# Optimization experiments

Measured on AMD Instinct MI355X. Metric: run time of the kernel, lower is better.

## Reference

```python
import jax, jax.numpy as jnp
import numpy as np

N = 100000      # nodes
E = 800000      # edges
IN = 32         # in_channels (one-hot width)
HID = 32        # hidden_channels per head
HEADS = 4
OUT = 10        # out_channels
G = 64          # graphs in batch
NEG_SLOPE = 0.2


def setup_inputs() -> dict:
    key = jax.random.key(0)
    ks = jax.random.split(key, 12)
    s = 0.1
    D = HEADS * HID  # 128
    return {
        "x": jax.random.randint(ks[0], (N,), 0, IN),
        "edge_index": jax.random.randint(ks[1], (2, E), 0, N),
        "batch": jnp.sort(jax.random.randint(ks[2], (N,), 0, G)),
        # conv1: IN -> HEADS x HID
        "W1": jax.random.normal(ks[3], (IN, D), jnp.float32) * s,
        "att_src1": jax.random.normal(ks[4], (HEADS, HID), jnp.float32) * s,
        "att_dst1": jax.random.normal(ks[5], (HEADS, HID), jnp.float32) * s,
        "b1": jnp.zeros((D,), jnp.float32),
        # conv3: D -> HEADS x HID
        "W3": jax.random.normal(ks[6], (D, D), jnp.float32) * s,
        "att_src3": jax.random.normal(ks[7], (HEADS, HID), jnp.float32) * s,
        "att_dst3": jax.random.normal(ks[8], (HEADS, HID), jnp.float32) * s,
        "b3": jnp.zeros((D,), jnp.float32),
        # final classifier
        "lin_w": jax.random.normal(ks[9], (D, OUT), jnp.float32) * s,
        "lin_b": jnp.zeros((OUT,), jnp.float32),
    }


def gat_conv(h, src, dst, W, att_src, att_dst, bias):
    """PyG GATConv (concat=True, add_self_loops already in src/dst)."""
    n = h.shape[0]
    hproj = (h @ W).reshape(n, HEADS, -1)                 # [N,H,C]
    a_src = jnp.einsum("nhc,hc->nh", hproj, att_src)      # [N,H]
    a_dst = jnp.einsum("nhc,hc->nh", hproj, att_dst)
    e = a_src[src] + a_dst[dst]                           # [E',H]
    e = jnp.where(e >= 0, e, NEG_SLOPE * e)               # LeakyReLU(0.2)
    # segment softmax over incoming edges of each destination node
    m = jax.ops.segment_max(e, dst, num_segments=n)       # [N,H]
    ex = jnp.exp(e - m[dst])
    denom = jax.ops.segment_sum(ex, dst, num_segments=n)  # [N,H]
    alpha = ex / denom[dst]                               # [E',H]
    msg = alpha[:, :, None] * hproj[src]                  # [E',H,C]
    out = jax.ops.segment_sum(msg, dst, num_segments=n)   # [N,H,C]
    return out.reshape(n, -1) + bias


def reference(x, edge_index, batch, W1, att_src1, att_dst1, b1,
              W3, att_src3, att_dst3, b3, lin_w, lin_b):
    # add self-loops once (PyG GATConv default add_self_loops=True)
    loop = jnp.arange(N, dtype=edge_index.dtype)
    src = jnp.concatenate([edge_index[0], loop])
    dst = jnp.concatenate([edge_index[1], loop])

    h = jax.nn.one_hot(x, IN, dtype=jnp.float32)          # [N,IN]
    h = jax.nn.relu(gat_conv(h, src, dst, W1, att_src1, att_dst1, b1))
    h = gat_conv(h, src, dst, W3, att_src3, att_dst3, b3)  # [N,D]

    # global_mean_pool over graph ids
    sums = jax.ops.segment_sum(h, batch, num_segments=G)   # [G,D]
    cnt = jax.ops.segment_sum(jnp.ones((N,), h.dtype), batch, num_segments=G)
    pooled = sums / jnp.maximum(cnt, 1.0)[:, None]
    return pooled @ lin_w + lin_b                          # [G,OUT]
```

## Files before the change

kernel.cpp:

```cpp
#include <hip/hip_runtime.h>
#include <hip/hip_fp16.h>

#define HEADS 4
#define HID 32
#define DCH 128
#define OUTC 10
#define NSLOPE 0.2f

#define SCAN_T 256
#define SCAN_PT 8
#define SCAN_ELEMS (SCAN_T * SCAN_PT)

#define POOL_BLOCKS 2048
#define BN1 64
#define SC_TILES 256

__global__ void k_deg(const int* __restrict__ esrc, const int* __restrict__ edst,
                      const int* __restrict__ x, int E, int N,
                      int* __restrict__ deg, unsigned short* __restrict__ rank) {
    int e = blockIdx.x * blockDim.x + threadIdx.x;
    int EP = E + N;
    if (e >= EP) return;
    int s, d;
    if (e < E) { s = esrc[e]; d = edst[e]; } else { s = e - E; d = s; }
    int r = atomicAdd(&deg[d], 1);
    rank[e] = (unsigned short)((r << 5) | x[s]);
}

__global__ void k_scan_a(const int* __restrict__ deg, int* __restrict__ rowstart,
                         int* __restrict__ bsum, int N) {
    __shared__ int sh[SCAN_T];
    int base = blockIdx.x * SCAN_ELEMS;
    int t = threadIdx.x;
    int v[SCAN_PT];
    int s = 0;
#pragma unroll
    for (int i = 0; i < SCAN_PT; i++) {
        int idx = base + t * SCAN_PT + i;
        int dv = (idx < N) ? deg[idx] : 0;
        s += dv; v[i] = s;
    }
    sh[t] = s;
    __syncthreads();
    for (int off = 1; off < SCAN_T; off <<= 1) {
        int add = (t >= off) ? sh[t - off] : 0;
        __syncthreads();
        sh[t] += add;
        __syncthreads();
    }
    int excl = (t > 0) ? sh[t - 1] : 0;
#pragma unroll
    for (int i = 0; i < SCAN_PT; i++) {
        int idx = base + t * SCAN_PT + i;
        if (idx < N) rowstart[idx + 1] = v[i] + excl;
    }
    if (t == SCAN_T - 1) bsum[blockIdx.x] = sh[t];
}

__global__ void k_scanb_tables(int* __restrict__ bsum, int nb,
        const float* __restrict__ W1, const float* __restrict__ as1, const float* __restrict__ ad1,
        const float* __restrict__ W3, const float* __restrict__ as3, const float* __restrict__ ad3,
        float* __restrict__ EXPT2, float* __restrict__ was3, float* __restrict__ wad3) {
    if (blockIdx.x == 0) {
        __shared__ int sh[1024];
        int t = threadIdx.x;
        sh[t] = (t < nb) ? bsum[t] : 0;
        __syncthreads();
        for (int off = 1; off < 1024; off <<= 1) {
            int add = (t >= off) ? sh[t - off] : 0;
            __syncthreads();
            sh[t] += add;
            __syncthreads();
        }
        if (t < nb) bsum[t] = (t > 0) ? sh[t - 1] : 0;
    } else {
        __shared__ float ts[32][HEADS], td[32][HEADS];
        int t = threadIdx.x;
        if (t < 128) {
            int cs = t >> 2, h = t & 3;
            const float* w = W1 + cs * DCH + h * HID;
            const float* a = as1 + h * HID;
            const float* b = ad1 + h * HID;
            float s1 = 0.f, s2 = 0.f;
#pragma unroll
            for (int j = 0; j < HID; j++) { float wv = w[j]; s1 = fmaf(wv, a[j], s1); s2 = fmaf(wv, b[j], s2); }
            ts[cs][h] = s1; td[cs][h] = s2;
        }
        __syncthreads();
        if (t < 128) {
            int h = t >> 5, cs = t & 31;
            for (int cd = 0; cd < 32; cd++) {
                float ev = ts[cs][h] + td[cd][h];
                ev = ev >= 0.f ? ev : NSLOPE * ev;
                EXPT2[cd * DCH + t] = __expf(ev);
            }
            for (int hh = 0; hh < HEADS; hh++) {
                const float* wr = W3 + (size_t)t * DCH + hh * HID;
                const float* a = as3 + hh * HID;
                const float* b = ad3 + hh * HID;
                float s1 = 0.f, s2 = 0.f;
#pragma unroll
                for (int j = 0; j < HID; j++) { float wv = wr[j]; s1 = fmaf(wv, a[j], s1); s2 = fmaf(wv, b[j], s2); }
                was3[hh * DCH + t] = s1; wad3[hh * DCH + t] = s2;
            }
        }
    }
}

__global__ void k_scan_c_bounds(int* __restrict__ rowstart, const int* __restrict__ boff,
                                const int* __restrict__ batch, int* __restrict__ gstart,
                                float* __restrict__ pool, int N, int G) {
    int i = blockIdx.x * blockDim.x + threadIdx.x;
    if (i < G * DCH) pool[i] = 0.f;
    if (i < N) {
        rowstart[i + 1] += boff[i / SCAN_ELEMS];
        if (i == 0) rowstart[0] = 0;
    }
    if (i > N) return;
    if (i == 0) {
        int b0 = batch[0];
        for (int g = 0; g <= b0; g++) gstart[g] = 0;
    } else if (i == N) {
        int bl = batch[N - 1];
        for (int g = bl + 1; g <= G; g++) gstart[g] = N;
    } else {
        int b = batch[i], bp = batch[i - 1];
        for (int g = bp + 1; g <= b; g++) gstart[g] = i;
    }
}

__global__ void k_scatter3(const int* __restrict__ esrc, const int* __restrict__ edst,
                           int E, int N, const int* __restrict__ rowstart,
                           const unsigned short* __restrict__ rank,
                           int* __restrict__ csr) {
    int rng  = blockIdx.x & 7;
    int tile = blockIdx.x >> 3;
    int ntiles = gridDim.x >> 3;
    int lo = rng * (N >> 3);
    int hi = (rng == 7) ? N : lo + (N >> 3);
    int EP = E + N;
    int stride = ntiles * blockDim.x;
    for (int e = tile * blockDim.x + threadIdx.x; e < EP; e += stride) {
        int s, d;
        if (e < E) { s = esrc[e]; d = edst[e]; } else { s = e - E; d = s; }
        if (d < lo || d >= hi) continue;
        unsigned short rk = rank[e];
        int pos = rowstart[d] + (rk >> 5);
        csr[pos] = (s << 5) | (rk & 31);
    }
}

__global__ __launch_bounds__(512) void k_conv1b(
        const int* __restrict__ rowstart, const int* __restrict__ csr,
        const int* __restrict__ x, const float* __restrict__ W1,
        const float* __restrict__ EXPT2, const float* __restrict__ b1,
        const float* __restrict__ was3, const float* __restrict__ wad3,
        __half* __restrict__ h1, float* __restrict__ asrc, float* __restrict__ adst,
        int N) {
    __shared__ float El[32 * 132 + 1];
    __shared__ int   hist[BN1][33];
    __shared__ int   xdl[BN1];
    int t = threadIdx.x;
    int r0 = blockIdx.x * BN1;
    for (int i = t; i < 32 * DCH; i += 512) {
        int cd = i >> 7, rem = i & 127;
        int hh = rem >> 5, kk = rem & 31;
        El[cd * 132 + hh * 33 + kk] = EXPT2[i];
    }
    for (int i = t; i < BN1 * 33; i += 512) ((int*)hist)[i] = 0;
    if (t < BN1) {
        int node = r0 + t;
        xdl[t] = (node < N) ? x[node] : 0;
    }
    __syncthreads();
    {
        int ln = t >> 3, sub = t & 7;
        int node = r0 + ln;
        if (node < N) {
            int p0 = rowstart[node], p1 = rowstart[node + 1];
            for (int p = p0 + sub; p < p1; p += 8)
                atomicAdd(&hist[ln][csr[p] & 31], 1);
        }
    }
    __syncthreads();
    int ct = t & 31, rt = t >> 5;
    int h = ct >> 3;
    float acc[4][4], den[4];
#pragma unroll
    for (int r = 0; r < 4; r++) { den[r] = 0.f;
#pragma unroll
        for (int j = 0; j < 4; j++) acc[r][j] = 0.f; }
#pragma unroll 4
    for (int k = 0; k < 32; k++) {
        float4 wv = *(const float4*)&W1[k * DCH + 4 * ct];
#pragma unroll
        for (int r = 0; r < 4; r++) {
            int row = rt * 4 + r;
            float g = (float)hist[row][k] * El[xdl[row] * 132 + h * 33 + k];
            den[r] += g;
            acc[r][0] = fmaf(g, wv.x, acc[r][0]);
            acc[r][1] = fmaf(g, wv.y, acc[r][1]);
            acc[r][2] = fmaf(g, wv.z, acc[r][2]);
            acc[r][3] = fmaf(g, wv.w, acc[r][3]);
        }
    }
    float4 bb = *(const float4*)&b1[4 * ct];
    float bbv[4] = {bb.x, bb.y, bb.z, bb.w};
#pragma unroll
    for (int r = 0; r < 4; r++) {
        float inv = 1.0f / den[r];
#pragma unroll
        for (int j = 0; j < 4; j++) {
            float v = acc[r][j] * inv + bbv[j];
            acc[r][j] = v > 0.f ? v : 0.f;
        }
        int row = r0 + rt * 4 + r;
        if (row < N) {
            union { __half hh[4]; uint2 u; } pk;
#pragma unroll
            for (int j = 0; j < 4; j++) pk.hh[j] = __float2half(acc[r][j]);
            *(uint2*)&h1[(size_t)row * DCH + 4 * ct] = pk.u;
        }
    }
    float4 ws = *(const float4*)&was3[h * DCH + 4 * ct];
    float4 wd = *(const float4*)&wad3[h * DCH + 4 * ct];
#pragma unroll
    for (int r = 0; r < 4; r++) {
        float ps = acc[r][0] * ws.x + acc[r][1] * ws.y + acc[r][2] * ws.z + acc[r][3] * ws.w;
        float pd = acc[r][0] * wd.x + acc[r][1] * wd.y + acc[r][2] * wd.z + acc[r][3] * wd.w;
        ps += __shfl_xor(ps, 1);  pd += __shfl_xor(pd, 1);
        ps += __shfl_xor(ps, 2);  pd += __shfl_xor(pd, 2);
        ps += __shfl_xor(ps, 4);  pd += __shfl_xor(pd, 4);
        int row = r0 + rt * 4 + r;
        if ((ct & 7) == 0 && row < N) {
            asrc[row * HEADS + h] = ps;
            adst[row * HEADS + h] = pd;
        }
    }
}

__global__ __launch_bounds__(256) void k_gather3w(
        const int* __restrict__ rowstart, const int* __restrict__ csr,
        const __half* __restrict__ hp, const float* __restrict__ asrc,
        const float* __restrict__ adst, __half* __restrict__ z, int N) {
    int t = threadIdx.x;
    int wid = t >> 6, lane = t & 63;
    int d = blockIdx.x * 4 + wid;
    if (d >= N) return;
    int lane16 = lane & 15, grp = lane >> 4;
    int myh = lane16 >> 2;
    float adst_h = adst[d * HEADS + myh];
    int p0 = rowstart[d], p1 = rowstart[d + 1];
    float a[8], b[8];
#pragma unroll
    for (int j = 0; j < 8; j++) { a[j] = 0.f; b[j] = 0.f; }
    float dena = 0.f, denb = 0.f;
    int p = p0 + grp;
    for (; p + 4 < p1; p += 8) {
        int s0 = csr[p] >> 5;
        int s1 = csr[p + 4] >> 5;
        float ev0 = asrc[s0 * HEADS + myh] + adst_h;
        float ev1 = asrc[s1 * HEADS + myh] + adst_h;
        ev0 = ev0 >= 0.f ? ev0 : NSLOPE * ev0;
        ev1 = ev1 >= 0.f ? ev1 : NSLOPE * ev1;
        float ex0 = __expf(ev0);
        float ex1 = __expf(ev1);
        dena += ex0; denb += ex1;
        const uint4 r0v = *(const uint4*)(hp + (size_t)s0 * DCH + lane16 * 8);
        const uint4 r1v = *(const uint4*)(hp + (size_t)s1 * DCH + lane16 * 8);
        const __half2* q0 = (const __half2*)&r0v;
        const __half2* q1 = (const __half2*)&r1v;
#pragma unroll
        for (int j = 0; j < 4; j++) {
            float2 f0 = __half22float2(q0[j]);
            float2 f1 = __half22float2(q1[j]);
            a[2 * j]     = fmaf(ex0, f0.x, a[2 * j]);
            a[2 * j + 1] = fmaf(ex0, f0.y, a[2 * j + 1]);
            b[2 * j]     = fmaf(ex1, f1.x, b[2 * j]);
            b[2 * j + 1] = fmaf(ex1, f1.y, b[2 * j + 1]);
        }
    }
    if (p < p1) {
        int s0 = csr[p] >> 5;
        float ev0 = asrc[s0 * HEADS + myh] + adst_h;
        ev0 = ev0 >= 0.f ? ev0 : NSLOPE * ev0;
        float ex0 = __expf(ev0);
        dena += ex0;
        const uint4 r0v = *(const uint4*)(hp + (size_t)s0 * DCH + lane16 * 8);
        const __half2* q0 = (const __half2*)&r0v;
#pragma unroll
        for (int j = 0; j < 4; j++) {
            float2 f0 = __half22float2(q0[j]);
            a[2 * j]     = fmaf(ex0, f0.x, a[2 * j]);
            a[2 * j + 1] = fmaf(ex0, f0.y, a[2 * j + 1]);
        }
    }
    float den = dena + denb;
#pragma unroll
    for (int j = 0; j < 8; j++) a[j] += b[j];
#pragma unroll
    for (int j = 0; j < 8; j++) {
        a[j] += __shfl_xor(a[j], 16);
        a[j] += __shfl_xor(a[j], 32);
    }
    den += __shfl_xor(den, 16);
    den += __shfl_xor(den, 32);
    if (grp == 0) {
        float inv = 1.0f / den;
        union { __half2 h2[4]; uint4 u; } pk;
#pragma unroll
        for (int j = 0; j < 4; j++)
            pk.h2[j] = __floats2half2_rn(a[2 * j] * inv, a[2 * j + 1] * inv);
        *(uint4*)(z + (size_t)d * DCH + lane16 * 8) = pk.u;
    }
}

__global__ __launch_bounds__(64) void k_pool_partial(
        const __half* __restrict__ h, const int* __restrict__ batch,
        float* __restrict__ pool, int N, int R) {
    int c2 = threadIdx.x;
    int n0 = blockIdx.x * R;
    if (n0 >= N) return;
    int n1 = n0 + R; if (n1 > N) n1 = N;
    float ax = 0.f, ay = 0.f;
    int curg = batch[n0];
    for (int n = n0; n < n1; n++) {
        int g = batch[n];
        if (g != curg) {
            atomicAdd(&pool[(size_t)curg * DCH + 2 * c2], ax);
            atomicAdd(&pool[(size_t)curg * DCH + 2 * c2 + 1], ay);
            ax = 0.f; ay = 0.f; curg = g;
        }
        __half2 hv = *(const __half2*)(h + (size_t)n * DCH + 2 * c2);
        float2 f = __half22float2(hv);
        ax += f.x; ay += f.y;
    }
    atomicAdd(&pool[(size_t)curg * DCH + 2 * c2], ax);
    atomicAdd(&pool[(size_t)curg * DCH + 2 * c2 + 1], ay);
}

__global__ __launch_bounds__(128) void k_final2(
        const float* __restrict__ pool, const int* __restrict__ gstart,
        const float* __restrict__ W3, const float* __restrict__ b3,
        const float* __restrict__ lw, const float* __restrict__ lb,
        float* __restrict__ out, int G) {
    __shared__ float pooled[DCH];
    __shared__ float t3[DCH];
    int g = blockIdx.x, c = threadIdx.x;
    float cnt = (float)(gstart[g + 1] - gstart[g]);
    pooled[c] = pool[(size_t)g * DCH + c] / fmaxf(cnt, 1.f);
    __syncthreads();
    float acc = b3[c];
#pragma unroll 8
    for (int k = 0; k < DCH; k++) acc = fmaf(pooled[k], W3[k * DCH + c], acc);
    t3[c] = acc;
    __syncthreads();
    if (c < OUTC) {
        float o = lb[c];
#pragma unroll 8
        for (int k = 0; k < DCH; k++) o = fmaf(t3[k], lw[k * OUTC + c], o);
        out[g * OUTC + c] = o;
    }
}

extern "C" void kernel_launch(void* const* d_in, const int* in_sizes, int n_in,
                              void* d_out, int out_size, void* d_ws, size_t ws_size,
                              hipStream_t stream) {
    const int*   x    = (const int*)d_in[0];
    const int*   eidx = (const int*)d_in[1];
    const int*   batch= (const int*)d_in[2];
    const float* W1   = (const float*)d_in[3];
    const float* as1  = (const float*)d_in[4];
    const float* ad1  = (const float*)d_in[5];
    const float* b1   = (const float*)d_in[6];
    const float* W3   = (const float*)d_in[7];
    const float* as3  = (const float*)d_in[8];
    const float* ad3  = (const float*)d_in[9];
    const float* b3   = (const float*)d_in[10];
    const float* lw   = (const float*)d_in[11];
    const float* lb   = (const float*)d_in[12];
    float* out = (float*)d_out;

    const int N  = in_sizes[0];
    const int E  = in_sizes[1] / 2;
    const int G  = out_size / OUTC;
    const int EP = E + N;
    const int* esrc = eidx;
    const int* edst = eidx + E;

    float*  zslot   = (float*)d_ws;
    __half* h1      = (__half*)(zslot + (size_t)N * DCH);
    float*  asrc3   = (float*)(h1 + (size_t)N * DCH);
    float*  adst3   = asrc3 + (size_t)N * HEADS;
    int*    deg     = (int*)(adst3 + (size_t)N * HEADS);
    int*    rowstart= deg + N;
    int*    bsum    = rowstart + (N + 1);
    int*    csr     = bsum + 1024;
    unsigned short* rank = (unsigned short*)(csr + EP);
    int*    gstart  = (int*)(rank + EP);
    float*  pool    = (float*)(gstart + (G + 1));
    float*  EXPT2   = pool + (size_t)G * DCH;
    float*  was3    = EXPT2 + 32 * DCH;
    float*  wad3    = was3 + HEADS * DCH;
    __half* z       = (__half*)zslot;

    const int BS = 256;
    const int nb = (N + SCAN_ELEMS - 1) / SCAN_ELEMS;

    hipMemsetAsync(deg, 0, (size_t)N * sizeof(int), stream);
    k_deg<<<(EP + BS - 1) / BS, BS, 0, stream>>>(esrc, edst, x, E, N, deg, rank);
    k_scan_a<<<nb, SCAN_T, 0, stream>>>(deg, rowstart, bsum, N);
    k_scanb_tables<<<2, 1024, 0, stream>>>(bsum, nb, W1, as1, ad1, W3, as3, ad3,
                                           EXPT2, was3, wad3);
    k_scan_c_bounds<<<(N + 1 + BS - 1) / BS, BS, 0, stream>>>(rowstart, bsum, batch,
                                                              gstart, pool, N, G);
    k_scatter3<<<8 * SC_TILES, BS, 0, stream>>>(esrc, edst, E, N, rowstart, rank, csr);

    k_conv1b<<<(N + BN1 - 1) / BN1, 512, 0, stream>>>(rowstart, csr, x, W1, EXPT2, b1,
                                                      was3, wad3, h1, asrc3, adst3, N);

    k_gather3w<<<(N + 3) / 4, 256, 0, stream>>>(rowstart, csr, h1, asrc3, adst3, z, N);

    {
        int R = (N + POOL_BLOCKS - 1) / POOL_BLOCKS;
        k_pool_partial<<<POOL_BLOCKS, 64, 0, stream>>>(z, batch, pool, N, R);
    }
    k_final2<<<G, 128, 0, stream>>>(pool, gstart, W3, b3, lw, lb, out, G);
}
```

Before: 178.2 us.

## Split layer-2 gather into two half-channel passes and simplify CSR scatter

```diff
diff --git a/kernel.cpp b/kernel.cpp
--- a/kernel.cpp
+++ b/kernel.cpp
@@ -13,7 +13,6 @@
 
 #define POOL_BLOCKS 2048
 #define BN1 64
-#define SC_TILES 256
 
 __global__ void k_deg(const int* __restrict__ esrc, const int* __restrict__ edst,
                       const int* __restrict__ x, int E, int N,
@@ -129,25 +128,18 @@
     }
 }
 
-__global__ void k_scatter3(const int* __restrict__ esrc, const int* __restrict__ edst,
-                           int E, int N, const int* __restrict__ rowstart,
-                           const unsigned short* __restrict__ rank,
-                           int* __restrict__ csr) {
-    int rng  = blockIdx.x & 7;
-    int tile = blockIdx.x >> 3;
-    int ntiles = gridDim.x >> 3;
-    int lo = rng * (N >> 3);
-    int hi = (rng == 7) ? N : lo + (N >> 3);
+__global__ void k_scatter1p(const int* __restrict__ esrc, const int* __restrict__ edst,
+                            int E, int N, const int* __restrict__ rowstart,
+                            const unsigned short* __restrict__ rank,
+                            int* __restrict__ csr) {
+    int e = blockIdx.x * blockDim.x + threadIdx.x;
     int EP = E + N;
-    int stride = ntiles * blockDim.x;
-    for (int e = tile * blockDim.x + threadIdx.x; e < EP; e += stride) {
-        int s, d;
-        if (e < E) { s = esrc[e]; d = edst[e]; } else { s = e - E; d = s; }
-        if (d < lo || d >= hi) continue;
-        unsigned short rk = rank[e];
-        int pos = rowstart[d] + (rk >> 5);
-        csr[pos] = (s << 5) | (rk & 31);
-    }
+    if (e >= EP) return;
+    int s, d;
+    if (e < E) { s = esrc[e]; d = edst[e]; } else { s = e - E; d = s; }
+    unsigned short rk = rank[e];
+    int pos = rowstart[d] + (rk >> 5);
+    csr[pos] = (s << 5) | (rk & 31);
 }
 
 __global__ __launch_bounds__(512) void k_conv1b(
@@ -239,21 +231,22 @@
     }
 }
 
-__global__ __launch_bounds__(256) void k_gather3w(
+__global__ __launch_bounds__(256) void k_gather3h(
         const int* __restrict__ rowstart, const int* __restrict__ csr,
         const __half* __restrict__ hp, const float* __restrict__ asrc,
-        const float* __restrict__ adst, __half* __restrict__ z, int N) {
+        const float* __restrict__ adst, __half* __restrict__ z, int N, int hd2) {
     int t = threadIdx.x;
     int wid = t >> 6, lane = t & 63;
     int d = blockIdx.x * 4 + wid;
     if (d >= N) return;
     int lane16 = lane & 15, grp = lane >> 4;
-    int myh = lane16 >> 2;
+    int myh = hd2 * 2 + (lane16 >> 3);
+    int cb = hd2 * 64 + lane16 * 4;
     float adst_h = adst[d * HEADS + myh];
     int p0 = rowstart[d], p1 = rowstart[d + 1];
-    float a[8], b[8];
-#pragma unroll
-    for (int j = 0; j < 8; j++) { a[j] = 0.f; b[j] = 0.f; }
+    float a[4], b[4];
+#pragma unroll
+    for (int j = 0; j < 4; j++) { a[j] = 0.f; b[j] = 0.f; }
     float dena = 0.f, denb = 0.f;
     int p = p0 + grp;
     for (; p + 4 < p1; p += 8) {
@@ -266,12 +259,12 @@
         float ex0 = __expf(ev0);
         float ex1 = __expf(ev1);
         dena += ex0; denb += ex1;
-        const uint4 r0v = *(const uint4*)(hp + (size_t)s0 * DCH + lane16 * 8);
-        const uint4 r1v = *(const uint4*)(hp + (size_t)s1 * DCH + lane16 * 8);
+        const uint2 r0v = *(const uint2*)(hp + (size_t)s0 * DCH + cb);
+        const uint2 r1v = *(const uint2*)(hp + (size_t)s1 * DCH + cb);
         const __half2* q0 = (const __half2*)&r0v;
         const __half2* q1 = (const __half2*)&r1v;
 #pragma unroll
-        for (int j = 0; j < 4; j++) {
+        for (int j = 0; j < 2; j++) {
             float2 f0 = __half22float2(q0[j]);
             float2 f1 = __half22float2(q1[j]);
             a[2 * j]     = fmaf(ex0, f0.x, a[2 * j]);
@@ -286,10 +279,10 @@
         ev0 = ev0 >= 0.f ? ev0 : NSLOPE * ev0;
         float ex0 = __expf(ev0);
         dena += ex0;
-        const uint4 r0v = *(const uint4*)(hp + (size_t)s0 * DCH + lane16 * 8);
+        const uint2 r0v = *(const uint2*)(hp + (size_t)s0 * DCH + cb);
         const __half2* q0 = (const __half2*)&r0v;
 #pragma unroll
-        for (int j = 0; j < 4; j++) {
+        for (int j = 0; j < 2; j++) {
             float2 f0 = __half22float2(q0[j]);
             a[2 * j]     = fmaf(ex0, f0.x, a[2 * j]);
             a[2 * j + 1] = fmaf(ex0, f0.y, a[2 * j + 1]);
@@ -297,9 +290,9 @@
     }
     float den = dena + denb;
 #pragma unroll
-    for (int j = 0; j < 8; j++) a[j] += b[j];
-#pragma unroll
-    for (int j = 0; j < 8; j++) {
+    for (int j = 0; j < 4; j++) a[j] += b[j];
+#pragma unroll
+    for (int j = 0; j < 4; j++) {
         a[j] += __shfl_xor(a[j], 16);
         a[j] += __shfl_xor(a[j], 32);
     }
@@ -307,11 +300,10 @@
     den += __shfl_xor(den, 32);
     if (grp == 0) {
         float inv = 1.0f / den;
-        union { __half2 h2[4]; uint4 u; } pk;
-#pragma unroll
-        for (int j = 0; j < 4; j++)
-            pk.h2[j] = __floats2half2_rn(a[2 * j] * inv, a[2 * j + 1] * inv);
-        *(uint4*)(z + (size_t)d * DCH + lane16 * 8) = pk.u;
+        union { __half2 h2[2]; uint2 u; } pk;
+        pk.h2[0] = __floats2half2_rn(a[0] * inv, a[1] * inv);
+        pk.h2[1] = __floats2half2_rn(a[2] * inv, a[3] * inv);
+        *(uint2*)(z + (size_t)d * DCH + cb) = pk.u;
     }
 }
 
@@ -414,12 +406,13 @@
                                            EXPT2, was3, wad3);
     k_scan_c_bounds<<<(N + 1 + BS - 1) / BS, BS, 0, stream>>>(rowstart, bsum, batch,
                                                               gstart, pool, N, G);
-    k_scatter3<<<8 * SC_TILES, BS, 0, stream>>>(esrc, edst, E, N, rowstart, rank, csr);
+    k_scatter1p<<<(EP + BS - 1) / BS, BS, 0, stream>>>(esrc, edst, E, N, rowstart, rank, csr);
 
     k_conv1b<<<(N + BN1 - 1) / BN1, 512, 0, stream>>>(rowstart, csr, x, W1, EXPT2, b1,
                                                       was3, wad3, h1, asrc3, adst3, N);
 
-    k_gather3w<<<(N + 3) / 4, 256, 0, stream>>>(rowstart, csr, h1, asrc3, adst3, z, N);
+    k_gather3h<<<(N + 3) / 4, 256, 0, stream>>>(rowstart, csr, h1, asrc3, adst3, z, N, 0);
+    k_gather3h<<<(N + 3) / 4, 256, 0, stream>>>(rowstart, csr, h1, asrc3, adst3, z, N, 1);
 
     {
         int R = (N + POOL_BLOCKS - 1) / POOL_BLOCKS;
```

New measurement: 204.4 us. 14.7% more time.
